# Optimization experiments

Hardware: AMD Instinct MI355X
Metric: run time of the kernel (lower is better)

## Reference

```python
import jax, jax.numpy as jnp
import numpy as np
from jax import lax

DIM = 64
HEADS = 8
B, H, W = 4, 256, 256


def layer_norm(x, w, b):
    # WithBias LayerNorm over channel dim (dim=1 of NCHW), per-pixel
    mu = jnp.mean(x, axis=1, keepdims=True)
    var = jnp.mean((x - mu) ** 2, axis=1, keepdims=True)
    xn = (x - mu) / jnp.sqrt(var + 1e-5)
    return xn * w[None, :, None, None] + b[None, :, None, None]


def conv1x1(x, w, b=None):
    out = jnp.einsum('oc,bchw->bohw', w, x)
    if b is not None:
        out = out + b[None, :, None, None]
    return out


def dwconv3x3(x, w):
    # w: [C,1,3,3], depthwise (groups=C), stride 1, pad 1
    return lax.conv_general_dilated(
        x, w, window_strides=(1, 1), padding=((1, 1), (1, 1)),
        feature_group_count=x.shape[1],
        dimension_numbers=('NCHW', 'OIHW', 'NCHW'))


def modulation(v, y, mw, mb):
    # mw: [4, C, C] = [scale0, scale1, shift0, shift1]; mb: [4, C]
    s = conv1x1(jax.nn.leaky_relu(conv1x1(y, mw[0], mb[0]), 0.1), mw[1], mb[1])
    t = conv1x1(jax.nn.leaky_relu(conv1x1(y, mw[2], mb[2]), 0.1), mw[3], mb[3])
    return v * (s + 1.0) + t


def _heads(t):
    b, c, h, w = t.shape
    return t.reshape(b, HEADS, c // HEADS, h * w)


def channel_attn(q, k, v, temp):
    b, c, h, w = v.shape
    q, k, v = _heads(q), _heads(k), _heads(v)  # b, head, ch, hw
    q = q / jnp.maximum(jnp.linalg.norm(q, axis=-1, keepdims=True), 1e-12)
    k = k / jnp.maximum(jnp.linalg.norm(k, axis=-1, keepdims=True), 1e-12)
    attn = jnp.einsum('bhcn,bhdn->bhcd', q, k) * temp[None]  # small CxC
    attn = jax.nn.softmax(attn, axis=-1)
    out = jnp.einsum('bhcd,bhdn->bhcn', attn, v)
    return out.reshape(b, c, h, w)


def setup_inputs() -> dict:
    key = jax.random.key(0)
    ks = jax.random.split(key, 24)
    sc = 0.05
    d = {
        'x': jax.random.normal(ks[0], (B, DIM, H, W), jnp.float32),
        'y': jax.random.normal(ks[1], (B, DIM, H, W), jnp.float32),
        'ln_w': jnp.ones((DIM,), jnp.float32),
        'ln_b': jnp.zeros((DIM,), jnp.float32),
        'temp': jnp.ones((HEADS, 1, 1), jnp.float32),
        'kv1_w': jax.random.normal(ks[2], (2 * DIM, DIM), jnp.float32) * sc,
        'kvdw1_w': jax.random.normal(ks[3], (2 * DIM, 1, 3, 3), jnp.float32) * sc,
        'q1_w': jax.random.normal(ks[4], (DIM, DIM), jnp.float32) * sc,
        'qdw1_w': jax.random.normal(ks[5], (DIM, 1, 3, 3), jnp.float32) * sc,
        'po1_w': jax.random.normal(ks[6], (DIM, DIM), jnp.float32) * sc,
        'kv2_w': jax.random.normal(ks[7], (2 * DIM, DIM), jnp.float32) * sc,
        'kvdw2_w': jax.random.normal(ks[8], (2 * DIM, 1, 3, 3), jnp.float32) * sc,
        'q2_w': jax.random.normal(ks[9], (DIM, DIM), jnp.float32) * sc,
        'qdw2_w': jax.random.normal(ks[10], (DIM, 1, 3, 3), jnp.float32) * sc,
        'po2_w': jax.random.normal(ks[11], (DIM, DIM), jnp.float32) * sc,
        'mm1_w': jax.random.normal(ks[12], (4, DIM, DIM), jnp.float32) * sc,
        'mm1_b': jnp.zeros((4, DIM), jnp.float32),
        'mm2_w': jax.random.normal(ks[13], (4, DIM, DIM), jnp.float32) * sc,
        'mm2_b': jnp.zeros((4, DIM), jnp.float32),
    }
    return d


def reference(x, y, ln_w, ln_b, temp,
              kv1_w, kvdw1_w, q1_w, qdw1_w, po1_w,
              kv2_w, kvdw2_w, q2_w, qdw2_w, po2_w,
              mm1_w, mm1_b, mm2_w, mm2_b):
    x1 = layer_norm(x, ln_w, ln_b)
    y1 = layer_norm(y, ln_w, ln_b)  # original reuses self.norm1 for both

    # branch 1: kv from x1, q from y1, v modulated by x, residual y
    kv1 = dwconv3x3(conv1x1(x1, kv1_w), kvdw1_w)
    k1, v1 = jnp.split(kv1, 2, axis=1)
    q1 = dwconv3x3(conv1x1(y1, q1_w), qdw1_w)
    v1 = modulation(v1, x, mm1_w, mm1_b)
    out1 = conv1x1(channel_attn(q1, k1, v1, temp), po1_w) + y

    # branch 2: kv from y1, q from x1, v modulated by y, residual x
    kv2 = dwconv3x3(conv1x1(y1, kv2_w), kvdw2_w)
    k2, v2 = jnp.split(kv2, 2, axis=1)
    q2 = dwconv3x3(conv1x1(x1, q2_w), qdw2_w)
    v2 = modulation(v2, y, mm2_w, mm2_b)
    out2 = conv1x1(channel_attn(q2, k2, v2, temp), po2_w) + x

    return (out1, out2)
```

## Files before the change

kernel.cpp:

```cpp
#include <hip/hip_runtime.h>
#include <hip/hip_bf16.h>

#define HW 65536
#define BATCH 4
#define NPIX (BATCH*HW)

typedef unsigned short u16;
typedef unsigned int   u32;
typedef __attribute__((ext_vector_type(8))) short bh8;
typedef __attribute__((ext_vector_type(4))) float f4;

__device__ __forceinline__ float b2f(u16 u){
    u32 i = ((u32)u) << 16; float f; __builtin_memcpy(&f, &i, 4); return f;
}
__device__ __forceinline__ u16 f2b(float f){
    __hip_bfloat16 h = __float2bfloat16(f); u16 u; __builtin_memcpy(&u, &h, 2); return u;
}

__device__ __forceinline__ f4 mfma16(bh8 a, bh8 b, f4 c){
    return __builtin_amdgcn_mfma_f32_16x16x32_bf16(a, b, c, 0, 0, 0);
}

struct CvtJob { const float* src; u16* dst; int n; const float* cs; };
struct SetupArgs {
    CvtJob j[12];
    const float* kvw[2]; const float* qw[2];
    const float* lnw; const float* lnb;
    float* sums; float* lnc;
};
__global__ __launch_bounds__(256) void setup_kernel(SetupArgs S){
    int blk = blockIdx.x;
    if (blk < 12){
        const CvtJob J = S.j[blk];
        if (J.cs){
            for (int i = threadIdx.x; i < J.n; i += 256) J.dst[i] = f2b(J.src[i] * J.cs[i & 63]);
        } else {
            for (int i = threadIdx.x; i < J.n; i += 256) J.dst[i] = f2b(J.src[i]);
        }
        return;
    }
    int pb = blk - 12;
    if (pb == 0){
        for (int i = threadIdx.x; i < 5120; i += 256) S.sums[i] = 0.f;
    } else if (pb <= 2){
        const float* W = S.kvw[pb-1];
        float* rs = S.lnc + (pb-1)*256;
        int o = threadIdx.x;
        if (o < 128){
            float a = 0.f, bb = 0.f;
            for (int c = 0; c < 64; c++){
                float wv = W[o*64 + c];
                a = fmaf(wv, S.lnw[c], a); bb = fmaf(wv, S.lnb[c], bb);
            }
            rs[o] = a; rs[128 + o] = bb;
        }
    } else {
        const float* W = S.qw[pb-3];
        float* rs = S.lnc + 512 + (pb-3)*128;
        int o = threadIdx.x;
        if (o < 64){
            float a = 0.f, bb = 0.f;
            for (int c = 0; c < 64; c++){
                float wv = W[o*64 + c];
                a = fmaf(wv, S.lnw[c], a); bb = fmaf(wv, S.lnb[c], bb);
            }
            rs[o] = a; rs[64 + o] = bb;
        }
    }
}

struct GemmDual {
    const float* in[2];
    const u16* wa[2];
    const float* rs[2]; const float* rb[2];
    u16* outLo[2]; u16* outHi[2];
};
template<int MT>
__global__ __launch_bounds__(256,4) void gemmln_kernel(GemmDual G){
    constexpr int KD = 64;
    constexpr int NW = MT*16*KD;
    __shared__ u16 wl[NW];
    int seg = blockIdx.x >> 11, tile = blockIdx.x & 2047;
    int w = threadIdx.x >> 6, lane = threadIdx.x & 63;
    int quad = lane >> 4, l16 = lane & 15;
    int b = tile >> 9;
    int pbase = ((tile & 511) << 7) + (w << 5) + (l16 << 1);

    const float* in = G.in[seg];
    float2 f[16];
    #pragma unroll
    for (int ks = 0; ks < 2; ks++)
        #pragma unroll
        for (int j = 0; j < 8; j++)
            f[ks*8+j] = *(const float2*)(in + ((size_t)b*64 + ks*32 + quad*8 + j)*HW + pbase);

    {
        const u16* W = G.wa[seg];
        for (int i = threadIdx.x; i < NW/8; i += 256){
            int row = i >> 3, ch = i & 7;
            uint4 v = *(const uint4*)(W + row*KD + ch*8);
            *(uint4*)(wl + row*KD + ((ch ^ (row & 7)) << 3)) = v;
        }
    }
    __syncthreads();

    float s1a = 0.f, s2a = 0.f, s1b = 0.f, s2b = 0.f;
    bh8 b0[2], b1[2];
    #pragma unroll
    for (int ks = 0; ks < 2; ks++)
        #pragma unroll
        for (int j = 0; j < 8; j++){
            float2 fv = f[ks*8+j];
            s1a += fv.x; s2a = fmaf(fv.x, fv.x, s2a);
            s1b += fv.y; s2b = fmaf(fv.y, fv.y, s2b);
            b0[ks][j] = (short)f2b(fv.x);
            b1[ks][j] = (short)f2b(fv.y);
        }

    f4 acc[MT][2];
    #pragma unroll
    for (int mi = 0; mi < MT; mi++){ acc[mi][0] = (f4){0.f,0.f,0.f,0.f}; acc[mi][1] = (f4){0.f,0.f,0.f,0.f}; }
    #pragma unroll
    for (int ks = 0; ks < 2; ks++)
        #pragma unroll
        for (int mi = 0; mi < MT; mi++){
            bh8 a;
            __builtin_memcpy(&a, wl + (mi*16 + l16)*KD + ((((ks<<2)+quad) ^ (l16 & 7)) << 3), 16);
            acc[mi][0] = mfma16(a, b0[ks], acc[mi][0]);
            acc[mi][1] = mfma16(a, b1[ks], acc[mi][1]);
        }

    s1a += __shfl_xor(s1a, 16); s1a += __shfl_xor(s1a, 32);
    s2a += __shfl_xor(s2a, 16); s2a += __shfl_xor(s2a, 32);
    s1b += __shfl_xor(s1b, 16); s1b += __shfl_xor(s1b, 32);
    s2b += __shfl_xor(s2b, 16); s2b += __shfl_xor(s2b, 32);
    float mu0 = s1a*(1.f/64.f), iv0 = rsqrtf(s2a*(1.f/64.f) - mu0*mu0 + 1e-5f);
    float mu1 = s1b*(1.f/64.f), iv1 = rsqrtf(s2b*(1.f/64.f) - mu1*mu1 + 1e-5f);

    const float* rs = G.rs[seg]; const float* rb = G.rb[seg];
    u16* oLo = G.outLo[seg]; u16* oHi = G.outHi[seg];
    #pragma unroll
    for (int mi = 0; mi < MT; mi++)
    #pragma unroll
    for (int r = 0; r < 4; r++){
        int o = mi*16 + quad*4 + r;
        size_t pidx = ((size_t)b*64 + (o & 63))*HW + pbase;
        float rsv = rs[o], rbv = rb[o];
        float va0 = iv0*(acc[mi][0][r] - mu0*rsv) + rbv;
        float va1 = iv1*(acc[mi][1][r] - mu1*rsv) + rbv;
        u16* dst = (o < 64) ? oLo : oHi;
        *(u32*)(dst + pidx) = (u32)f2b(va0) | ((u32)f2b(va1) << 16);
    }
}

struct Dw6 { const u16* in[6]; u16* out[6]; const float* w[6]; int choff[6]; };
__global__ __launch_bounds__(256) void dw6_kernel(Dw6 A){
    int seg = blockIdx.x >> 13;
    int lid = ((blockIdx.x & 8191) << 8) + threadIdx.x;
    const u16* inp = A.in[seg];
    u16* outp      = A.out[seg];
    const float* wd = A.w[seg];
    int choff      = A.choff[seg];
    int bc = lid >> 13;
    int n8 = lid & 8191;
    int h = n8 >> 5, c8 = (n8 & 31) << 3;
    const float* wc = wd + ((size_t)((bc & 63) + choff))*9;
    const u16* p = inp + (size_t)bc*HW;
    float row[3][10];
    #pragma unroll
    for (int r = 0; r < 3; r++){
        int hh = h - 1 + r;
        bool ok = (unsigned)hh < 256u;
        const u16* pr = p + hh*256 + c8;
        if (ok){
            uint4 m = *(const uint4*)pr;
            row[r][1] = b2f((u16)m.x); row[r][2] = b2f((u16)(m.x>>16));
            row[r][3] = b2f((u16)m.y); row[r][4] = b2f((u16)(m.y>>16));
            row[r][5] = b2f((u16)m.z); row[r][6] = b2f((u16)(m.z>>16));
            row[r][7] = b2f((u16)m.w); row[r][8] = b2f((u16)(m.w>>16));
            row[r][0] = (c8 > 0)   ? b2f(pr[-1]) : 0.f;
            row[r][9] = (c8 < 248) ? b2f(pr[8])  : 0.f;
        } else {
            #pragma unroll
            for (int j = 0; j < 10; j++) row[r][j] = 0.f;
        }
    }
    float o[8];
    #pragma unroll
    for (int i = 0; i < 8; i++){
        float a = 0.f;
        #pragma unroll
        for (int r = 0; r < 3; r++){
            a = fmaf(wc[r*3+0], row[r][i],   a);
            a = fmaf(wc[r*3+1], row[r][i+1], a);
            a = fmaf(wc[r*3+2], row[r][i+2], a);
        }
        o[i] = a;
    }
    uint4 st;
    st.x = (u32)f2b(o[0]) | ((u32)f2b(o[1])<<16);
    st.y = (u32)f2b(o[2]) | ((u32)f2b(o[3])<<16);
    st.z = (u32)f2b(o[4]) | ((u32)f2b(o[5])<<16);
    st.w = (u32)f2b(o[6]) | ((u32)f2b(o[7])<<16);
    *(uint4*)(outp + (size_t)bc*HW + h*256 + c8) = st;
}

#define NSL 64
struct AttnDual { const u16* q[2]; const u16* k[2]; float* sums; };
__global__ __launch_bounds__(256) void attn_part_kernel(AttnDual AD){
    int seg = blockIdx.x >> 11;
    int blk = blockIdx.x & 2047;
    int sl = blk & (NSL-1);
    int bh = blk >> 6;
    int b = bh >> 3, h = bh & 7;
    const u16* qp = AD.q[seg] + ((size_t)b*64 + h*8)*HW + sl*(HW/NSL);
    const u16* kp = AD.k[seg] + ((size_t)b*64 + h*8)*HW + sl*(HW/NSL);
    float acc[80];
    #pragma unroll
    for (int i = 0; i < 80; i++) acc[i] = 0.f;
    int n0 = threadIdx.x << 2;
    float qv[8][4], kw[8][4];
    #pragma unroll
    for (int i = 0; i < 8; i++){
        uint2 mq = *(const uint2*)(qp + (size_t)i*HW + n0);
        uint2 mk = *(const uint2*)(kp + (size_t)i*HW + n0);
        qv[i][0] = b2f((u16)(mq.x & 0xffffu)); qv[i][1] = b2f((u16)(mq.x >> 16));
        qv[i][2] = b2f((u16)(mq.y & 0xffffu)); qv[i][3] = b2f((u16)(mq.y >> 16));
        kw[i][0] = b2f((u16)(mk.x & 0xffffu)); kw[i][1] = b2f((u16)(mk.x >> 16));
        kw[i][2] = b2f((u16)(mk.y & 0xffffu)); kw[i][3] = b2f((u16)(mk.y >> 16));
    }
    #pragma unroll
    for (int i = 0; i < 8; i++){
        #pragma unroll
        for (int u = 0; u < 4; u++){
            acc[64+i] = fmaf(qv[i][u], qv[i][u], acc[64+i]);
            acc[72+i] = fmaf(kw[i][u], kw[i][u], acc[72+i]);
        }
        #pragma unroll
        for (int j = 0; j < 8; j++)
            #pragma unroll
            for (int u = 0; u < 4; u++)
                acc[i*8+j] = fmaf(qv[i][u], kw[j][u], acc[i*8+j]);
    }
    __shared__ float sred[4][80];
    int lane = threadIdx.x & 63, wv = threadIdx.x >> 6;
    #pragma unroll
    for (int t = 0; t < 80; t++){
        float r = acc[t];
        r += __shfl_down(r, 32); r += __shfl_down(r, 16); r += __shfl_down(r, 8);
        r += __shfl_down(r, 4);  r += __shfl_down(r, 2);  r += __shfl_down(r, 1);
        if (lane == 0) sred[wv][t] = r;
    }
    __syncthreads();
    if (threadIdx.x < 80){
        int t = threadIdx.x;
        atomicAdd(&AD.sums[seg*2560 + bh*80 + t], sred[0][t]+sred[1][t]+sred[2][t]+sred[3][t]);
    }
}

struct WeffDual { const float* sums; const float* temp; const float* po[2]; u16* weff[2]; };
__global__ __launch_bounds__(64) void weff_kernel(WeffDual WD){
    int seg = blockIdx.x >> 2;
    int b = blockIdx.x & 3;
    const float* po = WD.po[seg];
    u16* weff = WD.weff[seg];
    __shared__ float at[8][8][8];
    int t = threadIdx.x;
    {
        int h = t >> 3, i = t & 7;
        const float* f = WD.sums + seg*2560 + (b*8 + h)*80;
        float iq = 1.f / fmaxf(sqrtf(f[64+i]), 1e-12f);
        float tv = WD.temp[h];
        float row[8]; float m = -1e30f;
        #pragma unroll
        for (int j = 0; j < 8; j++){
            float ik = 1.f / fmaxf(sqrtf(f[72+j]), 1e-12f);
            row[j] = f[i*8+j]*iq*ik*tv;
            m = fmaxf(m, row[j]);
        }
        float s = 0.f;
        #pragma unroll
        for (int j = 0; j < 8; j++){ row[j] = expf(row[j]-m); s += row[j]; }
        float rsv = 1.f/s;
        #pragma unroll
        for (int j = 0; j < 8; j++) at[h][i][j] = row[j]*rsv;
    }
    __syncthreads();
    int o = t;
    for (int g = 0; g < 64; g++){
        int h = g >> 3, j = g & 7;
        float wv = 0.f;
        #pragma unroll
        for (int i = 0; i < 8; i++) wv = fmaf(po[o*64 + h*8 + i], at[h][i][j], wv);
        weff[b*4096 + o*64 + g] = f2b(wv);
    }
}

struct ModFinal {
    const float* in[2]; const u16* wa[2]; const u16* wb[2];
    const float* b0[2]; const float* b2[2]; const float* b1[2]; const float* b3[2];
    const u16* wf[2];
    const u16* v[2];
    const float* resid[2];
    float* out[2];
};
__global__ __launch_bounds__(256,4) void modfinal_kernel(ModFinal M){
    __shared__ u32 lds[128*64];
    int seg = blockIdx.x >> 11, tile = blockIdx.x & 2047;
    int w = threadIdx.x >> 6, lane = threadIdx.x & 63;
    int quad = lane >> 4, l16 = lane & 15;
    int b = tile >> 9;
    int pbase = ((tile & 511) << 7) + (w << 5) + (l16 << 1);
    int pxp = (w << 4) + l16;

    const float* in = M.in[seg];
    const u16* wa = M.wa[seg];

    float2 f[8];
    #pragma unroll
    for (int j = 0; j < 8; j++)
        f[j] = *(const float2*)(in + ((size_t)b*64 + quad*8 + j)*HW + pbase);

    f4 acc[8][2];
    #pragma unroll
    for (int mi = 0; mi < 8; mi++){ acc[mi][0] = (f4){0.f,0.f,0.f,0.f}; acc[mi][1] = (f4){0.f,0.f,0.f,0.f}; }

    #pragma unroll
    for (int ks = 0; ks < 2; ks++){
        float2 fn[8];
        if (ks == 0){
            #pragma unroll
            for (int j = 0; j < 8; j++)
                fn[j] = *(const float2*)(in + ((size_t)b*64 + 32 + quad*8 + j)*HW + pbase);
        }
        bh8 f0, f1;
        #pragma unroll
        for (int j = 0; j < 8; j++){
            f0[j] = (short)f2b(f[j].x);
            f1[j] = (short)f2b(f[j].y);
        }
        #pragma unroll
        for (int mi = 0; mi < 8; mi++){
            bh8 a;
            __builtin_memcpy(&a, wa + (mi*16 + l16)*64 + ks*32 + quad*8, 16);
            acc[mi][0] = mfma16(a, f0, acc[mi][0]);
            acc[mi][1] = mfma16(a, f1, acc[mi][1]);
        }
        #pragma unroll
        for (int j = 0; j < 8; j++) f[j] = fn[j];
    }

    u32 vpref[16];
    {
        const u16* vP = M.v[seg];
        #pragma unroll
        for (int mi = 0; mi < 4; mi++)
        #pragma unroll
        for (int r = 0; r < 4; r++)
            vpref[mi*4+r] = *(const u32*)(vP + ((size_t)b*64 + mi*16 + quad*4 + r)*HW + pbase);
    }

    {
        const float* b0v = M.b0[seg]; const float* b2v = M.b2[seg];
        #pragma unroll
        for (int mi = 0; mi < 8; mi++)
        #pragma unroll
        for (int r = 0; r < 4; r++){
            int o = mi*16 + quad*4 + r;
            float bi = (o < 64) ? b0v[o] : b2v[o-64];
            float v0 = acc[mi][0][r] + bi; v0 = v0 > 0.f ? v0 : 0.1f*v0;
            float v1 = acc[mi][1][r] + bi; v1 = v1 > 0.f ? v1 : 0.1f*v1;
            lds[o*64 + ((pxp + ((o>>2)&3)*8) & 63)] = (u32)f2b(v0) | ((u32)f2b(v1) << 16);
        }
    }
    __syncthreads();

    const u16* wb = M.wb[seg];
    f4 acc2[8][2];
    #pragma unroll
    for (int mi = 0; mi < 8; mi++){ acc2[mi][0] = (f4){0.f,0.f,0.f,0.f}; acc2[mi][1] = (f4){0.f,0.f,0.f,0.f}; }
    #pragma unroll
    for (int ks = 0; ks < 4; ks++){
        int kb = ks*32 + quad*8;
        bh8 bb0, bb1;
        #pragma unroll
        for (int j = 0; j < 8; j++){
            int ch = kb + j;
            u32 m = lds[ch*64 + ((pxp + ((ch>>2)&3)*8) & 63)];
            bb0[j] = (short)(m & 0xffffu);
            bb1[j] = (short)(m >> 16);
        }
        #pragma unroll
        for (int mi = 0; mi < 8; mi++){
            if (mi < 4 ? (ks < 2) : (ks >= 2)){
                int ksl = (mi >= 4) ? ks - 2 : ks;
                bh8 a;
                __builtin_memcpy(&a, wb + (mi*16 + l16)*64 + ksl*32 + quad*8, 16);
                acc2[mi][0] = mfma16(a, bb0, acc2[mi][0]);
                acc2[mi][1] = mfma16(a, bb1, acc2[mi][1]);
            }
        }
    }
    __syncthreads();

    {
        const float* b1v = M.b1[seg]; const float* b3v = M.b3[seg];
        #pragma unroll
        for (int mi = 0; mi < 4; mi++)
        #pragma unroll
        for (int r = 0; r < 4; r++){
            int o = mi*16 + quad*4 + r;
            float s0 = acc2[mi][0][r] + b1v[o];
            float s1 = acc2[mi][1][r] + b1v[o];
            float t0 = acc2[mi+4][0][r] + b3v[o];
            float t1 = acc2[mi+4][1][r] + b3v[o];
            u32 vv = vpref[mi*4+r];
            float v0 = b2f((u16)(vv & 0xffffu)), v1 = b2f((u16)(vv >> 16));
            lds[o*64 + ((pxp + ((o>>2)&3)*8) & 63)] = (u32)f2b(v0*(s0+1.f)+t0)
                                                    | ((u32)f2b(v1*(s1+1.f)+t1) << 16);
        }
    }
    float2 rpre[16];
    {
        const float* resid = M.resid[seg];
        #pragma unroll
        for (int mi = 0; mi < 4; mi++)
        #pragma unroll
        for (int r = 0; r < 4; r++)
            rpre[mi*4+r] = *(const float2*)(resid + ((size_t)b*64 + mi*16 + quad*4 + r)*HW + pbase);
    }
    __syncthreads();

    const u16* wf = M.wf[seg] + b*4096;
    f4 accF[4][2];
    #pragma unroll
    for (int mi = 0; mi < 4; mi++){ accF[mi][0] = (f4){0.f,0.f,0.f,0.f}; accF[mi][1] = (f4){0.f,0.f,0.f,0.f}; }
    #pragma unroll
    for (int ks = 0; ks < 2; ks++){
        int kb = ks*32 + quad*8;
        bh8 bb0, bb1;
        #pragma unroll
        for (int j = 0; j < 8; j++){
            int ch = kb + j;
            u32 m = lds[ch*64 + ((pxp + ((ch>>2)&3)*8) & 63)];
            bb0[j] = (short)(m & 0xffffu);
            bb1[j] = (short)(m >> 16);
        }
        #pragma unroll
        for (int mi = 0; mi < 4; mi++){
            bh8 a;
            __builtin_memcpy(&a, wf + (mi*16 + l16)*64 + ks*32 + quad*8, 16);
            accF[mi][0] = mfma16(a, bb0, accF[mi][0]);
            accF[mi][1] = mfma16(a, bb1, accF[mi][1]);
        }
    }
    {
        float* outF = M.out[seg];
        #pragma unroll
        for (int mi = 0; mi < 4; mi++)
        #pragma unroll
        for (int r = 0; r < 4; r++){
            int o = mi*16 + quad*4 + r;
            size_t pidx = ((size_t)b*64 + o)*HW + pbase;
            float2 rr = rpre[mi*4+r];
            float2 st; st.x = accF[mi][0][r] + rr.x; st.y = accF[mi][1][r] + rr.y;
            *(float2*)(outF + pidx) = st;
        }
    }
}

extern "C" void kernel_launch(void* const* d_in, const int* in_sizes, int n_in,
                              void* d_out, int out_size, void* d_ws, size_t ws_size,
                              hipStream_t stream){
    const float* x    = (const float*)d_in[0];
    const float* y    = (const float*)d_in[1];
    const float* ln_w = (const float*)d_in[2];
    const float* ln_b = (const float*)d_in[3];
    const float* temp = (const float*)d_in[4];
    const float* kv_w[2]   = {(const float*)d_in[5],  (const float*)d_in[10]};
    const float* kvdw_w[2] = {(const float*)d_in[6],  (const float*)d_in[11]};
    const float* q_w[2]    = {(const float*)d_in[7],  (const float*)d_in[12]};
    const float* qdw_w[2]  = {(const float*)d_in[8],  (const float*)d_in[13]};
    const float* po_w[2]   = {(const float*)d_in[9],  (const float*)d_in[14]};
    const float* mm_w[2]   = {(const float*)d_in[15], (const float*)d_in[17]};
    const float* mm_b[2]   = {(const float*)d_in[16], (const float*)d_in[18]};

    const size_t HPE = (size_t)BATCH*64*HW;
    u16* PL = (u16*)d_ws;
    u16* P[12];
    for (int i = 0; i < 12; i++) P[i] = PL + (size_t)i*HPE;
    float* sums = (float*)(PL + 12*HPE);
    float* lnc  = sums + 5120;
    u16* warena = (u16*)(lnc + 768);
    const int WKV[2] = {0, 8192}, WQ[2] = {16384, 20480};
    const int WMA[2] = {24576, 40960}, WMB[2] = {32768, 49152};
    const int WEFF[2] = {57344, 73728};

    size_t need = 12*HPE*2 + (5120+768)*4 + 90112*2;
    if (ws_size < need) return;

    SetupArgs S{};
    int nj = 0;
    auto add = [&](const float* s, u16* d, int n, const float* cs){ S.j[nj] = {s, d, n, cs}; nj++; };
    for (int br = 0; br < 2; br++){
        add(kv_w[br],        warena + WKV[br],        8192, ln_w);
        add(q_w[br],         warena + WQ[br],         4096, ln_w);
        add(mm_w[br],        warena + WMA[br],        4096, nullptr);
        add(mm_w[br]+8192,   warena + WMA[br] + 4096, 4096, nullptr);
        add(mm_w[br]+4096,   warena + WMB[br],        4096, nullptr);
        add(mm_w[br]+12288,  warena + WMB[br] + 4096, 4096, nullptr);
    }
    S.kvw[0] = kv_w[0]; S.kvw[1] = kv_w[1];
    S.qw[0]  = q_w[0];  S.qw[1]  = q_w[1];
    S.lnw = ln_w; S.lnb = ln_b; S.sums = sums; S.lnc = lnc;
    setup_kernel<<<17, 256, 0, stream>>>(S);

    const int GT = NPIX/128;

    GemmDual GK{};
    GK.in[0] = x; GK.in[1] = y;
    GK.wa[0] = warena + WKV[0]; GK.wa[1] = warena + WKV[1];
    GK.rs[0] = lnc;        GK.rb[0] = lnc + 128;
    GK.rs[1] = lnc + 256;  GK.rb[1] = lnc + 384;
    GK.outLo[0] = P[0]; GK.outHi[0] = P[1];
    GK.outLo[1] = P[2]; GK.outHi[1] = P[3];
    gemmln_kernel<8><<<2*GT, 256, 0, stream>>>(GK);

    GemmDual GQ{};
    GQ.in[0] = y; GQ.in[1] = x;
    GQ.wa[0] = warena + WQ[0]; GQ.wa[1] = warena + WQ[1];
    GQ.rs[0] = lnc + 512;  GQ.rb[0] = lnc + 576;
    GQ.rs[1] = lnc + 640;  GQ.rb[1] = lnc + 704;
    GQ.outLo[0] = P[4]; GQ.outHi[0] = P[4];
    GQ.outLo[1] = P[5]; GQ.outHi[1] = P[5];
    gemmln_kernel<4><<<2*GT, 256, 0, stream>>>(GQ);

    Dw6 D{};
    D.in[0] = P[0];  D.out[0] = P[6];  D.w[0] = kvdw_w[0]; D.choff[0] = 0;
    D.in[1] = P[1];  D.out[1] = P[7];  D.w[1] = kvdw_w[0]; D.choff[1] = 64;
    D.in[2] = P[4];  D.out[2] = P[8];  D.w[2] = qdw_w[0];  D.choff[2] = 0;
    D.in[3] = P[2];  D.out[3] = P[9];  D.w[3] = kvdw_w[1]; D.choff[3] = 0;
    D.in[4] = P[3];  D.out[4] = P[10]; D.w[4] = kvdw_w[1]; D.choff[4] = 64;
    D.in[5] = P[5];  D.out[5] = P[11]; D.w[5] = qdw_w[1];  D.choff[5] = 0;
    dw6_kernel<<<6*8192, 256, 0, stream>>>(D);

    AttnDual AD{};
    AD.q[0] = P[8];  AD.k[0] = P[6];
    AD.q[1] = P[11]; AD.k[1] = P[9];
    AD.sums = sums;
    attn_part_kernel<<<2*BATCH*8*NSL, 256, 0, stream>>>(AD);

    WeffDual WD{};
    WD.sums = sums; WD.temp = temp;
    WD.po[0] = po_w[0]; WD.po[1] = po_w[1];
    WD.weff[0] = warena + WEFF[0]; WD.weff[1] = warena + WEFF[1];
    weff_kernel<<<2*BATCH, 64, 0, stream>>>(WD);

    float* outp = (float*)d_out;
    ModFinal M{};
    M.in[0] = x; M.in[1] = y;
    M.wa[0] = warena + WMA[0]; M.wa[1] = warena + WMA[1];
    M.wb[0] = warena + WMB[0]; M.wb[1] = warena + WMB[1];
    M.b0[0] = mm_b[0];       M.b0[1] = mm_b[1];
    M.b2[0] = mm_b[0] + 128; M.b2[1] = mm_b[1] + 128;
    M.b1[0] = mm_b[0] + 64;  M.b1[1] = mm_b[1] + 64;
    M.b3[0] = mm_b[0] + 192; M.b3[1] = mm_b[1] + 192;
    M.wf[0] = warena + WEFF[0]; M.wf[1] = warena + WEFF[1];
    M.v[0] = P[7]; M.v[1] = P[10];
    M.resid[0] = y; M.resid[1] = x;
    M.out[0] = outp; M.out[1] = outp + HPE;
    modfinal_kernel<<<2*GT, 256, 0, stream>>>(M);
}
```

Measured before the change: 721.4 us.

## Process four pixels per lane in gemmln and modfinal kernels with wider tiles

Doubles the pixel tile per block from 128 to 256 in the LayerNorm-GEMM and modulation/final kernels, so each lane handles four adjacent pixels with 16-byte float4 loads and wider packed stores. Each weight fragment loaded from LDS or global memory is reused across four MFMAs instead of two, and the grid is halved. In exchange, accumulator and register pressure doubles, the occupancy hint in launch bounds is dropped, and modfinal's LDS use grows to 64KB per block, which may reduce occupancy.

```diff
diff --git a/kernel.cpp b/kernel.cpp
--- a/kernel.cpp
+++ b/kernel.cpp
@@ -76,23 +76,21 @@
     u16* outLo[2]; u16* outHi[2];
 };
 template<int MT>
-__global__ __launch_bounds__(256,4) void gemmln_kernel(GemmDual G){
+__global__ __launch_bounds__(256) void gemmln_kernel(GemmDual G){
     constexpr int KD = 64;
     constexpr int NW = MT*16*KD;
     __shared__ u16 wl[NW];
-    int seg = blockIdx.x >> 11, tile = blockIdx.x & 2047;
+    int seg = blockIdx.x >> 10, tile = blockIdx.x & 1023;
     int w = threadIdx.x >> 6, lane = threadIdx.x & 63;
     int quad = lane >> 4, l16 = lane & 15;
-    int b = tile >> 9;
-    int pbase = ((tile & 511) << 7) + (w << 5) + (l16 << 1);
+    int b = tile >> 8;
+    int pbase = ((tile & 255) << 8) + (w << 6) + (l16 << 2);
 
     const float* in = G.in[seg];
-    float2 f[16];
-    #pragma unroll
-    for (int ks = 0; ks < 2; ks++)
-        #pragma unroll
-        for (int j = 0; j < 8; j++)
-            f[ks*8+j] = *(const float2*)(in + ((size_t)b*64 + ks*32 + quad*8 + j)*HW + pbase);
+    f4 fin[8];
+    #pragma unroll
+    for (int j = 0; j < 8; j++)
+        fin[j] = *(const f4*)(in + ((size_t)b*64 + quad*8 + j)*HW + pbase);
 
     {
         const u16* W = G.wa[seg];
@@ -104,38 +102,49 @@
     }
     __syncthreads();
 
-    float s1a = 0.f, s2a = 0.f, s1b = 0.f, s2b = 0.f;
-    bh8 b0[2], b1[2];
-    #pragma unroll
-    for (int ks = 0; ks < 2; ks++)
+    f4 fin2[8];
+    #pragma unroll
+    for (int j = 0; j < 8; j++)
+        fin2[j] = *(const f4*)(in + ((size_t)b*64 + 32 + quad*8 + j)*HW + pbase);
+
+    float s1[4] = {0.f,0.f,0.f,0.f}, s2[4] = {0.f,0.f,0.f,0.f};
+    f4 acc[MT][4];
+    #pragma unroll
+    for (int mi = 0; mi < MT; mi++)
+        #pragma unroll
+        for (int p = 0; p < 4; p++) acc[mi][p] = (f4){0.f,0.f,0.f,0.f};
+
+    #pragma unroll
+    for (int ks = 0; ks < 2; ks++){
+        bh8 bfr[4];
         #pragma unroll
         for (int j = 0; j < 8; j++){
-            float2 fv = f[ks*8+j];
-            s1a += fv.x; s2a = fmaf(fv.x, fv.x, s2a);
-            s1b += fv.y; s2b = fmaf(fv.y, fv.y, s2b);
-            b0[ks][j] = (short)f2b(fv.x);
-            b1[ks][j] = (short)f2b(fv.y);
-        }
-
-    f4 acc[MT][2];
-    #pragma unroll
-    for (int mi = 0; mi < MT; mi++){ acc[mi][0] = (f4){0.f,0.f,0.f,0.f}; acc[mi][1] = (f4){0.f,0.f,0.f,0.f}; }
-    #pragma unroll
-    for (int ks = 0; ks < 2; ks++)
+            f4 fv = (ks == 0) ? fin[j] : fin2[j];
+            #pragma unroll
+            for (int p = 0; p < 4; p++){
+                float v = fv[p];
+                s1[p] += v; s2[p] = fmaf(v, v, s2[p]);
+                bfr[p][j] = (short)f2b(v);
+            }
+        }
         #pragma unroll
         for (int mi = 0; mi < MT; mi++){
             bh8 a;
             __builtin_memcpy(&a, wl + (mi*16 + l16)*KD + ((((ks<<2)+quad) ^ (l16 & 7)) << 3), 16);
-            acc[mi][0] = mfma16(a, b0[ks], acc[mi][0]);
-            acc[mi][1] = mfma16(a, b1[ks], acc[mi][1]);
-        }
-
-    s1a += __shfl_xor(s1a, 16); s1a += __shfl_xor(s1a, 32);
-    s2a += __shfl_xor(s2a, 16); s2a += __shfl_xor(s2a, 32);
-    s1b += __shfl_xor(s1b, 16); s1b += __shfl_xor(s1b, 32);
-    s2b += __shfl_xor(s2b, 16); s2b += __shfl_xor(s2b, 32);
-    float mu0 = s1a*(1.f/64.f), iv0 = rsqrtf(s2a*(1.f/64.f) - mu0*mu0 + 1e-5f);
-    float mu1 = s1b*(1.f/64.f), iv1 = rsqrtf(s2b*(1.f/64.f) - mu1*mu1 + 1e-5f);
+            #pragma unroll
+            for (int p = 0; p < 4; p++)
+                acc[mi][p] = mfma16(a, bfr[p], acc[mi][p]);
+        }
+    }
+
+    float mu[4], iv[4];
+    #pragma unroll
+    for (int p = 0; p < 4; p++){
+        s1[p] += __shfl_xor(s1[p], 16); s1[p] += __shfl_xor(s1[p], 32);
+        s2[p] += __shfl_xor(s2[p], 16); s2[p] += __shfl_xor(s2[p], 32);
+        mu[p] = s1[p]*(1.f/64.f);
+        iv[p] = rsqrtf(s2[p]*(1.f/64.f) - mu[p]*mu[p] + 1e-5f);
+    }
 
     const float* rs = G.rs[seg]; const float* rb = G.rb[seg];
     u16* oLo = G.outLo[seg]; u16* oHi = G.outHi[seg];
@@ -146,10 +155,15 @@
         int o = mi*16 + quad*4 + r;
         size_t pidx = ((size_t)b*64 + (o & 63))*HW + pbase;
         float rsv = rs[o], rbv = rb[o];
-        float va0 = iv0*(acc[mi][0][r] - mu0*rsv) + rbv;
-        float va1 = iv1*(acc[mi][1][r] - mu1*rsv) + rbv;
+        float v0 = iv[0]*(acc[mi][0][r] - mu[0]*rsv) + rbv;
+        float v1 = iv[1]*(acc[mi][1][r] - mu[1]*rsv) + rbv;
+        float v2 = iv[2]*(acc[mi][2][r] - mu[2]*rsv) + rbv;
+        float v3 = iv[3]*(acc[mi][3][r] - mu[3]*rsv) + rbv;
+        uint2 st;
+        st.x = (u32)f2b(v0) | ((u32)f2b(v1) << 16);
+        st.y = (u32)f2b(v2) | ((u32)f2b(v3) << 16);
         u16* dst = (o < 64) ? oLo : oHi;
-        *(u32*)(dst + pidx) = (u32)f2b(va0) | ((u32)f2b(va1) << 16);
+        *(uint2*)(dst + pidx) = st;
     }
 }
 
@@ -304,60 +318,59 @@
     const float* resid[2];
     float* out[2];
 };
-__global__ __launch_bounds__(256,4) void modfinal_kernel(ModFinal M){
-    __shared__ u32 lds[128*64];
-    int seg = blockIdx.x >> 11, tile = blockIdx.x & 2047;
+__global__ __launch_bounds__(256) void modfinal_kernel(ModFinal M){
+    __shared__ u32 lds[128*128];
+    int seg = blockIdx.x >> 10, tile = blockIdx.x & 1023;
     int w = threadIdx.x >> 6, lane = threadIdx.x & 63;
     int quad = lane >> 4, l16 = lane & 15;
-    int b = tile >> 9;
-    int pbase = ((tile & 511) << 7) + (w << 5) + (l16 << 1);
-    int pxp = (w << 4) + l16;
+    int b = tile >> 8;
+    int pbase = ((tile & 255) << 8) + (w << 6) + (l16 << 2);
+    int pp = ((w << 4) + l16) << 1;
 
     const float* in = M.in[seg];
     const u16* wa = M.wa[seg];
 
-    float2 f[8];
+    f4 fin[8], fin2[8];
     #pragma unroll
     for (int j = 0; j < 8; j++)
-        f[j] = *(const float2*)(in + ((size_t)b*64 + quad*8 + j)*HW + pbase);
-
-    f4 acc[8][2];
-    #pragma unroll
-    for (int mi = 0; mi < 8; mi++){ acc[mi][0] = (f4){0.f,0.f,0.f,0.f}; acc[mi][1] = (f4){0.f,0.f,0.f,0.f}; }
+        fin[j] = *(const f4*)(in + ((size_t)b*64 + quad*8 + j)*HW + pbase);
+    #pragma unroll
+    for (int j = 0; j < 8; j++)
+        fin2[j] = *(const f4*)(in + ((size_t)b*64 + 32 + quad*8 + j)*HW + pbase);
+
+    f4 acc[8][4];
+    #pragma unroll
+    for (int mi = 0; mi < 8; mi++)
+        #pragma unroll
+        for (int p = 0; p < 4; p++) acc[mi][p] = (f4){0.f,0.f,0.f,0.f};
 
     #pragma unroll
     for (int ks = 0; ks < 2; ks++){
-        float2 fn[8];
-        if (ks == 0){
-            #pragma unroll
-            for (int j = 0; j < 8; j++)
-                fn[j] = *(const float2*)(in + ((size_t)b*64 + 32 + quad*8 + j)*HW + pbase);
-        }
-        bh8 f0, f1;
+        bh8 bfr[4];
         #pragma unroll
         for (int j = 0; j < 8; j++){
-            f0[j] = (short)f2b(f[j].x);
-            f1[j] = (short)f2b(f[j].y);
+            f4 fv = (ks == 0) ? fin[j] : fin2[j];
+            #pragma unroll
+            for (int p = 0; p < 4; p++) bfr[p][j] = (short)f2b(fv[p]);
         }
         #pragma unroll
         for (int mi = 0; mi < 8; mi++){
             bh8 a;
             __builtin_memcpy(&a, wa + (mi*16 + l16)*64 + ks*32 + quad*8, 16);
-            acc[mi][0] = mfma16(a, f0, acc[mi][0]);
-            acc[mi][1] = mfma16(a, f1, acc[mi][1]);
-        }
-        #pragma unroll
-        for (int j = 0; j < 8; j++) f[j] = fn[j];
-    }
-
-    u32 vpref[16];
+            #pragma unroll
+            for (int p = 0; p < 4; p++)
+                acc[mi][p] = mfma16(a, bfr[p], acc[mi][p]);
+        }
+    }
+
+    uint2 vpref[16];
     {
         const u16* vP = M.v[seg];
         #pragma unroll
         for (int mi = 0; mi < 4; mi++)
         #pragma unroll
         for (int r = 0; r < 4; r++)
-            vpref[mi*4+r] = *(const u32*)(vP + ((size_t)b*64 + mi*16 + quad*4 + r)*HW + pbase);
+            vpref[mi*4+r] = *(const uint2*)(vP + ((size_t)b*64 + mi*16 + quad*4 + r)*HW + pbase);
     }
 
     {
@@ -370,25 +383,34 @@
             float bi = (o < 64) ? b0v[o] : b2v[o-64];
             float v0 = acc[mi][0][r] + bi; v0 = v0 > 0.f ? v0 : 0.1f*v0;
             float v1 = acc[mi][1][r] + bi; v1 = v1 > 0.f ? v1 : 0.1f*v1;
-            lds[o*64 + ((pxp + ((o>>2)&3)*8) & 63)] = (u32)f2b(v0) | ((u32)f2b(v1) << 16);
+            float v2 = acc[mi][2][r] + bi; v2 = v2 > 0.f ? v2 : 0.1f*v2;
+            float v3 = acc[mi][3][r] + bi; v3 = v3 > 0.f ? v3 : 0.1f*v3;
+            uint2 st;
+            st.x = (u32)f2b(v0) | ((u32)f2b(v1) << 16);
+            st.y = (u32)f2b(v2) | ((u32)f2b(v3) << 16);
+            *(uint2*)&lds[o*128 + ((pp + ((o>>2)&3)*8) & 127)] = st;
         }
     }
     __syncthreads();
 
     const u16* wb = M.wb[seg];
-    f4 acc2[8][2];
-    #pragma unroll
-    for (int mi = 0; mi < 8; mi++){ acc2[mi][0] = (f4){0.f,0.f,0.f,0.f}; acc2[mi][1] = (f4){0.f,0.f,0.f,0.f}; }
+    f4 acc2[8][4];
+    #pragma unroll
+    for (int mi = 0; mi < 8; mi++)
+        #pragma unroll
+        for (int p = 0; p < 4; p++) acc2[mi][p] = (f4){0.f,0.f,0.f,0.f};
     #pragma unroll
     for (int ks = 0; ks < 4; ks++){
         int kb = ks*32 + quad*8;
-        bh8 bb0, bb1;
+        bh8 bfr[4];
         #pragma unroll
         for (int j = 0; j < 8; j++){
             int ch = kb + j;
-            u32 m = lds[ch*64 + ((pxp + ((ch>>2)&3)*8) & 63)];
-            bb0[j] = (short)(m & 0xffffu);
-            bb1[j] = (short)(m >> 16);
+            uint2 m = *(const uint2*)&lds[ch*128 + ((pp + ((ch>>2)&3)*8) & 127)];
+            bfr[0][j] = (short)(m.x & 0xffffu);
+            bfr[1][j] = (short)(m.x >> 16);
+            bfr[2][j] = (short)(m.y & 0xffffu);
+            bfr[3][j] = (short)(m.y >> 16);
         }
         #pragma unroll
         for (int mi = 0; mi < 8; mi++){
@@ -396,8 +418,9 @@
                 int ksl = (mi >= 4) ? ks - 2 : ks;
                 bh8 a;
                 __builtin_memcpy(&a, wb + (mi*16 + l16)*64 + ksl*32 + quad*8, 16);
-                acc2[mi][0] = mfma16(a, bb0, acc2[mi][0]);
-                acc2[mi][1] = mfma16(a, bb1, acc2[mi][1]);
+                #pragma unroll
+                for (int p = 0; p < 4; p++)
+                    acc2[mi][p] = mfma16(a, bfr[p], acc2[mi][p]);
             }
         }
     }
@@ -410,48 +433,59 @@
         #pragma unroll
         for (int r = 0; r < 4; r++){
             int o = mi*16 + quad*4 + r;
-            float s0 = acc2[mi][0][r] + b1v[o];
-            float s1 = acc2[mi][1][r] + b1v[o];
-            float t0 = acc2[mi+4][0][r] + b3v[o];
-            float t1 = acc2[mi+4][1][r] + b3v[o];
-            u32 vv = vpref[mi*4+r];
-            float v0 = b2f((u16)(vv & 0xffffu)), v1 = b2f((u16)(vv >> 16));
-            lds[o*64 + ((pxp + ((o>>2)&3)*8) & 63)] = (u32)f2b(v0*(s0+1.f)+t0)
-                                                    | ((u32)f2b(v1*(s1+1.f)+t1) << 16);
-        }
-    }
-    float2 rpre[16];
+            uint2 vv = vpref[mi*4+r];
+            float va[4] = { b2f((u16)(vv.x & 0xffffu)), b2f((u16)(vv.x >> 16)),
+                            b2f((u16)(vv.y & 0xffffu)), b2f((u16)(vv.y >> 16)) };
+            float ov[4];
+            #pragma unroll
+            for (int p = 0; p < 4; p++){
+                float s = acc2[mi][p][r] + b1v[o];
+                float t = acc2[mi+4][p][r] + b3v[o];
+                ov[p] = va[p]*(s+1.f)+t;
+            }
+            uint2 st;
+            st.x = (u32)f2b(ov[0]) | ((u32)f2b(ov[1]) << 16);
+            st.y = (u32)f2b(ov[2]) | ((u32)f2b(ov[3]) << 16);
+            *(uint2*)&lds[o*128 + ((pp + ((o>>2)&3)*8) & 127)] = st;
+        }
+    }
+    f4 rpre[16];
     {
         const float* resid = M.resid[seg];
         #pragma unroll
         for (int mi = 0; mi < 4; mi++)
         #pragma unroll
         for (int r = 0; r < 4; r++)
-            rpre[mi*4+r] = *(const float2*)(resid + ((size_t)b*64 + mi*16 + quad*4 + r)*HW + pbase);
+            rpre[mi*4+r] = *(const f4*)(resid + ((size_t)b*64 + mi*16 + quad*4 + r)*HW + pbase);
     }
     __syncthreads();
 
     const u16* wf = M.wf[seg] + b*4096;
-    f4 accF[4][2];
-    #pragma unroll
-    for (int mi = 0; mi < 4; mi++){ accF[mi][0] = (f4){0.f,0.f,0.f,0.f}; accF[mi][1] = (f4){0.f,0.f,0.f,0.f}; }
+    f4 accF[4][4];
+    #pragma unroll
+    for (int mi = 0; mi < 4; mi++)
+        #pragma unroll
+        for (int p = 0; p < 4; p++) accF[mi][p] = (f4){0.f,0.f,0.f,0.f};
     #pragma unroll
     for (int ks = 0; ks < 2; ks++){
         int kb = ks*32 + quad*8;
-        bh8 bb0, bb1;
+        bh8 bfr[4];
         #pragma unroll
         for (int j = 0; j < 8; j++){
             int ch = kb + j;
-            u32 m = lds[ch*64 + ((pxp + ((ch>>2)&3)*8) & 63)];
-            bb0[j] = (short)(m & 0xffffu);
-            bb1[j] = (short)(m >> 16);
+            uint2 m = *(const uint2*)&lds[ch*128 + ((pp + ((ch>>2)&3)*8) & 127)];
+            bfr[0][j] = (short)(m.x & 0xffffu);
+            bfr[1][j] = (short)(m.x >> 16);
+            bfr[2][j] = (short)(m.y & 0xffffu);
+            bfr[3][j] = (short)(m.y >> 16);
         }
         #pragma unroll
         for (int mi = 0; mi < 4; mi++){
             bh8 a;
             __builtin_memcpy(&a, wf + (mi*16 + l16)*64 + ks*32 + quad*8, 16);
-            accF[mi][0] = mfma16(a, bb0, accF[mi][0]);
-            accF[mi][1] = mfma16(a, bb1, accF[mi][1]);
+            #pragma unroll
+            for (int p = 0; p < 4; p++)
+                accF[mi][p] = mfma16(a, bfr[p], accF[mi][p]);
         }
     }
     {
@@ -462,9 +496,11 @@
         for (int r = 0; r < 4; r++){
             int o = mi*16 + quad*4 + r;
             size_t pidx = ((size_t)b*64 + o)*HW + pbase;
-            float2 rr = rpre[mi*4+r];
-            float2 st; st.x = accF[mi][0][r] + rr.x; st.y = accF[mi][1][r] + rr.y;
-            *(float2*)(outF + pidx) = st;
+            f4 rr = rpre[mi*4+r];
+            f4 st;
+            #pragma unroll
+            for (int p = 0; p < 4; p++) st[p] = accF[mi][p][r] + rr[p];
+            *(f4*)(outF + pidx) = st;
         }
     }
 }
@@ -515,7 +551,7 @@
     S.lnw = ln_w; S.lnb = ln_b; S.sums = sums; S.lnc = lnc;
     setup_kernel<<<17, 256, 0, stream>>>(S);
 
-    const int GT = NPIX/128;
+    const int GT = NPIX/256;
 
     GemmDual GK{};
     GK.in[0] = x; GK.in[1] = y;
```

Measured after the change: 694.8 us. 3.7% less time.
